# Kernel tuning notes

Hardware: AMD Instinct MI355X
Metric: run time of the kernel (lower is better)

## Reference

```python
import jax, jax.numpy as jnp
import numpy as np

N, E, D = 50000, 1000000, 64
EPS = 1e-5


def setup_inputs() -> dict:
    key = jax.random.key(0)
    ks = jax.random.split(key, 20)
    inp = {
        "x": jax.random.normal(ks[0], (N, D), dtype=jnp.float32),
        "e": jax.random.uniform(ks[1], (E,), dtype=jnp.float32),
        "edge_index": jax.random.randint(ks[2], (2, E), 0, N, dtype=jnp.int64),
    }
    dims = [(3 * D, D), (D, D), (D, D), (D, D)]
    for i, (fi, fo) in enumerate(dims):
        s = 1.0 / np.sqrt(fi)
        inp[f"W{i+1}"] = jax.random.uniform(ks[3 + 4 * i], (fi, fo), minval=-s, maxval=s, dtype=jnp.float32)
        inp[f"b{i+1}"] = jax.random.uniform(ks[4 + 4 * i], (fo,), minval=-s, maxval=s, dtype=jnp.float32)
        inp[f"g{i+1}"] = jnp.ones((fo,), dtype=jnp.float32)
        inp[f"bt{i+1}"] = jnp.zeros((fo,), dtype=jnp.float32)
    return inp


def _layer(h, W, b, g, bt):
    h = h @ W + b
    mu = jnp.mean(h, axis=-1, keepdims=True)
    var = jnp.mean(jnp.square(h - mu), axis=-1, keepdims=True)
    h = (h - mu) * jax.lax.rsqrt(var + EPS) * g + bt
    return jax.nn.relu(h)


def reference(x, e, edge_index, W1, b1, g1, bt1, W2, b2, g2, bt2, W3, b3, g3, bt3, W4, b4, g4, bt4):
    start, end = edge_index[0], edge_index[1]
    we = e[:, None]  # [E,1]
    # aggregate weighted neighbor features on each side
    mi = jax.ops.segment_sum(we * x[start], end, num_segments=x.shape[0])
    mo = jax.ops.segment_sum(we * x[end], start, num_segments=x.shape[0])
    h = jnp.concatenate([mi, mo, x], axis=1)  # [N, 3D]
    h = _layer(h, W1, b1, g1, bt1)
    h = _layer(h, W2, b2, g2, bt2)
    h = _layer(h, W3, b3, g3, bt3)
    h = _layer(h, W4, b4, g4, bt4)
    return h
```

## Files before the change

### kernel.cpp

```cpp
#include <hip/hip_runtime.h>

#define DD 64
#define EPSV 1e-5f

__device__ __forceinline__ float rlane_f(float v, int k) {
    return __int_as_float(__builtin_amdgcn_readlane(__float_as_int(v), k));
}

__global__ void detect_idx_kernel(const void* __restrict__ idx, int* __restrict__ flag,
                                  int nsample, int n_nodes) {
    const long long* p = (const long long*)idx;
    int bad = 0;
    for (int i = threadIdx.x; i < nsample; i += blockDim.x) {
        long long v = p[i];
        if (v < 0 || v >= (long long)n_nodes) bad = 1;
    }
    __shared__ int sbad;
    if (threadIdx.x == 0) sbad = 0;
    __syncthreads();
    if (bad) atomicOr(&sbad, 1);
    __syncthreads();
    if (threadIdx.x == 0) *flag = sbad ? 0 : 1;
}

__global__ __launch_bounds__(256) void hist_kernel(
    const void* __restrict__ idx, const int* __restrict__ flag,
    int* __restrict__ cnt0, int* __restrict__ cnt1, int n_edges) {
    const bool is64 = (*flag != 0);
    const long long* p64 = (const long long*)idx;
    const int*       p32 = (const int*)idx;
    int tid = blockIdx.x * blockDim.x + threadIdx.x;
    int stride = gridDim.x * blockDim.x;
    for (int ed = tid; ed < n_edges; ed += stride) {
        int s, t;
        if (is64) { s = (int)p64[ed]; t = (int)p64[n_edges + ed]; }
        else      { s = p32[ed];      t = p32[n_edges + ed]; }
        atomicAdd(&cnt0[t], 1);
        atomicAdd(&cnt1[s], 1);
    }
}

#define SC 52
__global__ __launch_bounds__(1024) void scan_kernel(
    const int* __restrict__ cnt0, const int* __restrict__ cnt1,
    int* __restrict__ offs0, int* __restrict__ offs1,
    int* __restrict__ cur0, int* __restrict__ cur1, int n) {
    const int* cnt = blockIdx.x ? cnt1 : cnt0;
    int* offs = blockIdx.x ? offs1 : offs0;
    int* cur  = blockIdx.x ? cur1  : cur0;
    const int t = threadIdx.x;
    const int base = t * SC;
    int m = n - base; if (m > SC) m = SC; if (m < 0) m = 0;

    int v[SC];
    int sum = 0;
    if (m == SC) {
        const int4* c4 = (const int4*)(cnt + base);
        #pragma unroll
        for (int i = 0; i < SC / 4; ++i) {
            int4 q = c4[i];
            v[4*i] = q.x; v[4*i+1] = q.y; v[4*i+2] = q.z; v[4*i+3] = q.w;
        }
        #pragma unroll
        for (int i = 0; i < SC; ++i) sum += v[i];
    } else {
        for (int i = 0; i < m; ++i) sum += cnt[base + i];
    }

    const int lane = t & 63, wid = t >> 6;
    int s = sum;
    #pragma unroll
    for (int d = 1; d < 64; d <<= 1) { int u = __shfl_up(s, d, 64); if (lane >= d) s += u; }

    __shared__ int wtot[16];
    if (lane == 63) wtot[wid] = s;
    __syncthreads();
    if (t < 16) {
        int w = wtot[t];
        int sw = w;
        #pragma unroll
        for (int d = 1; d < 16; d <<= 1) { int u = __shfl_up(sw, d, 64); if (t >= d) sw += u; }
        wtot[t] = sw - w;
    }
    __syncthreads();

    int run = wtot[wid] + (s - sum);
    if (m == SC) {
        int4* o4 = (int4*)(offs + base);
        int4* c4w = (int4*)(cur + base);
        #pragma unroll
        for (int i = 0; i < SC / 4; ++i) {
            int4 q;
            q.x = run; run += v[4*i];
            q.y = run; run += v[4*i+1];
            q.z = run; run += v[4*i+2];
            q.w = run; run += v[4*i+3];
            o4[i] = q; c4w[i] = q;
        }
        if (base + SC == n) offs[n] = run;
    } else if (m > 0) {
        for (int i = 0; i < m; ++i) {
            int c = cnt[base + i];
            offs[base + i] = run;
            cur[base + i]  = run;
            run += c;
        }
        if (base + m == n) offs[n] = run;
    }
}

__global__ __launch_bounds__(256) void fill_kernel(
    const void* __restrict__ idx, const float* __restrict__ e, const int* __restrict__ flag,
    int* __restrict__ cur0, int* __restrict__ cur1,
    int2* __restrict__ pay0, int2* __restrict__ pay1, int n_edges) {
    const bool is64 = (*flag != 0);
    const long long* p64 = (const long long*)idx;
    const int*       p32 = (const int*)idx;
    int tid = blockIdx.x * blockDim.x + threadIdx.x;
    int stride = gridDim.x * blockDim.x;
    for (int ed = tid; ed < n_edges; ed += stride) {
        int s, t;
        if (is64) { s = (int)p64[ed]; t = (int)p64[n_edges + ed]; }
        else      { s = p32[ed];      t = p32[n_edges + ed]; }
        int wbits = __float_as_int(e[ed]);
        int p0 = atomicAdd(&cur0[t], 1);
        pay0[p0] = make_int2(s, wbits);
        int p1 = atomicAdd(&cur1[s], 1);
        pay1[p1] = make_int2(t, wbits);
    }
}

__global__ __launch_bounds__(256) void gather_kernel(
    const float* __restrict__ x,
    const int2* __restrict__ pay0, const int2* __restrict__ pay1,
    const int* __restrict__ offs0, const int* __restrict__ offs1,
    float* __restrict__ mi, float* __restrict__ mo, int n) {
    const int wid = threadIdx.x >> 6, lane = threadIdx.x & 63;
    const int gid = blockIdx.x * 4 + wid;
    if (gid >= 2 * n) return;
    const int dir = gid & 1, node = gid >> 1;
    const int* offs = dir ? offs1 : offs0;
    const int2* pay = dir ? pay1 : pay0;
    float* dst = dir ? mo : mi;

    const int o0 = offs[node], o1 = offs[node + 1];
    float acc = 0.0f;
    for (int b = o0; b < o1; b += 64) {
        int2 pl = make_int2(0, 0);
        if (b + lane < o1) pl = pay[b + lane];
        const int cnt = min(64, o1 - b);
        #pragma unroll 4
        for (int j = 0; j < cnt; ++j) {
            int src  = __builtin_amdgcn_readlane(pl.x, j);
            float w  = __int_as_float(__builtin_amdgcn_readlane(pl.y, j));
            acc = fmaf(w, x[src * DD + lane], acc);
        }
    }
    dst[node * DD + lane] = acc;
}

__global__ __launch_bounds__(256) void scatter_kernel(
    const float* __restrict__ x, const float* __restrict__ e,
    const void* __restrict__ idx, const int* __restrict__ flag,
    float* __restrict__ mi, float* __restrict__ mo, int n_edges) {
    const int lane  = threadIdx.x & 63;
    const int slot  = (blockIdx.x * blockDim.x + threadIdx.x) >> 6;
    const int nslot = (gridDim.x * blockDim.x) >> 6;
    const bool is64 = (*flag != 0);
    const long long* p64 = (const long long*)idx;
    const int*       p32 = (const int*)idx;
    for (int ed = slot; ed < n_edges; ed += nslot) {
        int s, t;
        if (is64) { s = (int)p64[ed]; t = (int)p64[n_edges + ed]; }
        else      { s = p32[ed];      t = p32[n_edges + ed]; }
        float w  = e[ed];
        unsafeAtomicAdd(&mi[t * DD + lane], w * x[s * DD + lane]);
        unsafeAtomicAdd(&mo[s * DD + lane], w * x[t * DD + lane]);
    }
}

#define NPW 13

template<int N>
__device__ __forceinline__ void accumG(const float* __restrict__ wcol,
                                       const float (&h)[N], float (&acc)[N]) {
    #pragma unroll 8
    for (int k = 0; k < 64; ++k) {
        float w = wcol[k * 64];
        #pragma unroll
        for (int m = 0; m < N; ++m) acc[m] = fmaf(w, rlane_f(h[m], k), acc[m]);
    }
}

__device__ __forceinline__ float ln_relu(float v, float g, float bt) {
    float s = v;
    #pragma unroll
    for (int off = 32; off; off >>= 1) s += __shfl_xor(s, off, 64);
    float mu = s * (1.0f / 64.0f);
    float d = v - mu;
    float s2 = d * d;
    #pragma unroll
    for (int off = 32; off; off >>= 1) s2 += __shfl_xor(s2, off, 64);
    float r = d * rsqrtf(s2 * (1.0f / 64.0f) + EPSV) * g + bt;
    return fmaxf(r, 0.0f);
}

__global__ __launch_bounds__(512) void fused_mlp4(
    const float* __restrict__ mi, const float* __restrict__ mo, const float* __restrict__ x,
    const float* __restrict__ W1, const float* __restrict__ b1, const float* __restrict__ g1, const float* __restrict__ bt1,
    const float* __restrict__ W2, const float* __restrict__ b2, const float* __restrict__ g2, const float* __restrict__ bt2,
    const float* __restrict__ W3, const float* __restrict__ b3, const float* __restrict__ g3, const float* __restrict__ bt3,
    const float* __restrict__ W4, const float* __restrict__ b4, const float* __restrict__ g4, const float* __restrict__ bt4,
    float* __restrict__ out, int n_nodes) {

    const int wid = threadIdx.x >> 6, lane = threadIdx.x & 63;
    const int gw = blockIdx.x * 8 + wid;
    const int ngroups = (n_nodes + NPW - 1) / NPW;
    if (gw >= ngroups) return;
    const int n0 = gw * NPW;

    float hmi[NPW], hmo[NPW], hx[NPW];
    #pragma unroll
    for (int m = 0; m < NPW; ++m) {
        int n = n0 + m; if (n >= n_nodes) n = n_nodes - 1;
        hmi[m] = mi[n * DD + lane];
        hmo[m] = mo[n * DD + lane];
        hx[m]  = x[n * DD + lane];
    }

    float acc[NPW], h[NPW];

    {
        float bj = b1[lane];
        #pragma unroll
        for (int m = 0; m < NPW; ++m) acc[m] = bj;
        accumG(W1 + lane,             hmi, acc);
        accumG(W1 + 64 * DD + lane,   hmo, acc);
        accumG(W1 + 128 * DD + lane,  hx,  acc);
        float gj = g1[lane], btj = bt1[lane];
        #pragma unroll
        for (int m = 0; m < NPW; ++m) h[m] = ln_relu(acc[m], gj, btj);
    }

    {
        float bj = b2[lane];
        #pragma unroll
        for (int m = 0; m < NPW; ++m) acc[m] = bj;
        accumG(W2 + lane, h, acc);
        float gj = g2[lane], btj = bt2[lane];
        #pragma unroll
        for (int m = 0; m < NPW; ++m) h[m] = ln_relu(acc[m], gj, btj);
    }
    {
        float bj = b3[lane];
        #pragma unroll
        for (int m = 0; m < NPW; ++m) acc[m] = bj;
        accumG(W3 + lane, h, acc);
        float gj = g3[lane], btj = bt3[lane];
        #pragma unroll
        for (int m = 0; m < NPW; ++m) h[m] = ln_relu(acc[m], gj, btj);
    }
    {
        float bj = b4[lane];
        #pragma unroll
        for (int m = 0; m < NPW; ++m) acc[m] = bj;
        accumG(W4 + lane, h, acc);
        float gj = g4[lane], btj = bt4[lane];
        #pragma unroll
        for (int m = 0; m < NPW; ++m) h[m] = ln_relu(acc[m], gj, btj);
    }

    #pragma unroll
    for (int m = 0; m < NPW; ++m) {
        int n = n0 + m;
        if (n < n_nodes) out[n * DD + lane] = h[m];
    }
}

extern "C" void kernel_launch(void* const* d_in, const int* in_sizes, int n_in,
                              void* d_out, int out_size, void* d_ws, size_t ws_size,
                              hipStream_t stream) {
    const float* x   = (const float*)d_in[0];
    const float* e   = (const float*)d_in[1];
    const void*  idx = d_in[2];
    const float* W1 = (const float*)d_in[3],  *b1 = (const float*)d_in[4],
               * g1 = (const float*)d_in[5],  *bt1 = (const float*)d_in[6];
    const float* W2 = (const float*)d_in[7],  *b2 = (const float*)d_in[8],
               * g2 = (const float*)d_in[9],  *bt2 = (const float*)d_in[10];
    const float* W3 = (const float*)d_in[11], *b3 = (const float*)d_in[12],
               * g3 = (const float*)d_in[13], *bt3 = (const float*)d_in[14];
    const float* W4 = (const float*)d_in[15], *b4 = (const float*)d_in[16],
               * g4 = (const float*)d_in[17], *bt4 = (const float*)d_in[18];
    float* out = (float*)d_out;

    const int n_nodes = in_sizes[0] / DD;
    const int n_edges = in_sizes[1];

    float* mi = (float*)d_ws;
    float* mo = mi + (size_t)n_nodes * DD;
    int*  flag = (int*)(mo + (size_t)n_nodes * DD);
    char* p = (char*)(flag + 4);
    const int offs_pad = (n_nodes + 1 + 3) & ~3;
    int2* pay0 = (int2*)p;            p += (size_t)n_edges * sizeof(int2);
    int2* pay1 = (int2*)p;            p += (size_t)n_edges * sizeof(int2);
    int* cnt0  = (int*)p;             p += (size_t)n_nodes * 4;
    int* cnt1  = (int*)p;             p += (size_t)n_nodes * 4;
    int* offs0 = (int*)p;             p += (size_t)offs_pad * 4;
    int* offs1 = (int*)p;             p += (size_t)offs_pad * 4;
    int* cur0  = (int*)p;             p += (size_t)n_nodes * 4;
    int* cur1  = (int*)p;             p += (size_t)n_nodes * 4;
    const size_t need = (size_t)(p - (char*)d_ws);

    detect_idx_kernel<<<1, 256, 0, stream>>>(idx, flag, 4096, n_nodes);

    if (ws_size >= need) {
        hipMemsetAsync(cnt0, 0, (size_t)2 * n_nodes * 4, stream);
        hist_kernel<<<2048, 256, 0, stream>>>(idx, flag, cnt0, cnt1, n_edges);
        scan_kernel<<<2, 1024, 0, stream>>>(cnt0, cnt1, offs0, offs1, cur0, cur1, n_nodes);
        fill_kernel<<<2048, 256, 0, stream>>>(idx, e, flag, cur0, cur1, pay0, pay1, n_edges);
        const int nblocks = (2 * n_nodes + 3) / 4;
        gather_kernel<<<nblocks, 256, 0, stream>>>(x, pay0, pay1, offs0, offs1, mi, mo, n_nodes);
    } else {
        hipMemsetAsync(d_ws, 0, (size_t)2 * n_nodes * DD * sizeof(float), stream);
        scatter_kernel<<<4096, 256, 0, stream>>>(x, e, idx, flag, mi, mo, n_edges);
    }

    const int ngroups = (n_nodes + NPW - 1) / NPW;
    const int mblocks = (ngroups + 7) / 8;
    fused_mlp4<<<mblocks, 512, 0, stream>>>(
        mi, mo, x,
        W1, b1, g1, bt1, W2, b2, g2, bt2, W3, b3, g3, bt3, W4, b4, g4, bt4,
        out, n_nodes);
}
```

Measured before the change: 604.3 us.

## Replace per-node CSR build with coarse node bins and LDS atomic accumulation

Edges are bucketed into bins of 256 destination nodes, with a shared-memory histogram, a tiny scan, and an atomic append into one payload array carrying the local node index. Each bin is then reduced by a workgroup into a 64KB LDS tile using shared-memory float atomics and written out. This removes the per-node scan and the per-node counters, but it adds heavy global atomic contention on a few hundred bin cursors and LDS atomic traffic. The 64KB LDS tile limits occupancy, and summation order becomes nondeterministic.

```diff
diff --git a/kernel.cpp b/kernel.cpp
--- a/kernel.cpp
+++ b/kernel.cpp
@@ -2,6 +2,8 @@
 
 #define DD 64
 #define EPSV 1e-5f
+#define BINSZ 256
+#define NBINMAX 256
 
 __device__ __forceinline__ float rlane_f(float v, int k) {
     return __int_as_float(__builtin_amdgcn_readlane(__float_as_int(v), k));
@@ -23,140 +25,109 @@
     if (threadIdx.x == 0) *flag = sbad ? 0 : 1;
 }
 
-__global__ __launch_bounds__(256) void hist_kernel(
+__global__ __launch_bounds__(512) void binhist_kernel(
     const void* __restrict__ idx, const int* __restrict__ flag,
-    int* __restrict__ cnt0, int* __restrict__ cnt1, int n_edges) {
+    int* __restrict__ cnt, int nbin, int n_edges) {
+    __shared__ int h[2 * NBINMAX];
+    const int tid = threadIdx.x;
+    for (int i = tid; i < 2 * nbin; i += 512) h[i] = 0;
+    __syncthreads();
     const bool is64 = (*flag != 0);
     const long long* p64 = (const long long*)idx;
     const int*       p32 = (const int*)idx;
-    int tid = blockIdx.x * blockDim.x + threadIdx.x;
-    int stride = gridDim.x * blockDim.x;
-    for (int ed = tid; ed < n_edges; ed += stride) {
+    int gid = blockIdx.x * 512 + tid;
+    int stride = gridDim.x * 512;
+    for (int ed = gid; ed < n_edges; ed += stride) {
         int s, t;
         if (is64) { s = (int)p64[ed]; t = (int)p64[n_edges + ed]; }
         else      { s = p32[ed];      t = p32[n_edges + ed]; }
-        atomicAdd(&cnt0[t], 1);
-        atomicAdd(&cnt1[s], 1);
-    }
-}
-
-#define SC 52
-__global__ __launch_bounds__(1024) void scan_kernel(
-    const int* __restrict__ cnt0, const int* __restrict__ cnt1,
-    int* __restrict__ offs0, int* __restrict__ offs1,
-    int* __restrict__ cur0, int* __restrict__ cur1, int n) {
-    const int* cnt = blockIdx.x ? cnt1 : cnt0;
-    int* offs = blockIdx.x ? offs1 : offs0;
-    int* cur  = blockIdx.x ? cur1  : cur0;
+        atomicAdd(&h[t >> 8], 1);
+        atomicAdd(&h[nbin + (s >> 8)], 1);
+    }
+    __syncthreads();
+    for (int i = tid; i < 2 * nbin; i += 512) {
+        int v = h[i];
+        if (v) atomicAdd(&cnt[i], v);
+    }
+}
+
+__global__ void binscan_kernel(const int* __restrict__ cnt,
+                               int* __restrict__ base, int* __restrict__ cur, int nb) {
     const int t = threadIdx.x;
-    const int base = t * SC;
-    int m = n - base; if (m > SC) m = SC; if (m < 0) m = 0;
-
-    int v[SC];
+    const int C = (nb + 63) >> 6;
+    const int b0 = t * C;
+    int m = nb - b0; if (m > C) m = C; if (m < 0) m = 0;
+    int v[8];
     int sum = 0;
-    if (m == SC) {
-        const int4* c4 = (const int4*)(cnt + base);
-        #pragma unroll
-        for (int i = 0; i < SC / 4; ++i) {
-            int4 q = c4[i];
-            v[4*i] = q.x; v[4*i+1] = q.y; v[4*i+2] = q.z; v[4*i+3] = q.w;
-        }
-        #pragma unroll
-        for (int i = 0; i < SC; ++i) sum += v[i];
-    } else {
-        for (int i = 0; i < m; ++i) sum += cnt[base + i];
-    }
-
-    const int lane = t & 63, wid = t >> 6;
+    for (int i = 0; i < m; ++i) { v[i] = cnt[b0 + i]; sum += v[i]; }
     int s = sum;
     #pragma unroll
-    for (int d = 1; d < 64; d <<= 1) { int u = __shfl_up(s, d, 64); if (lane >= d) s += u; }
-
-    __shared__ int wtot[16];
-    if (lane == 63) wtot[wid] = s;
-    __syncthreads();
-    if (t < 16) {
-        int w = wtot[t];
-        int sw = w;
-        #pragma unroll
-        for (int d = 1; d < 16; d <<= 1) { int u = __shfl_up(sw, d, 64); if (t >= d) sw += u; }
-        wtot[t] = sw - w;
-    }
-    __syncthreads();
-
-    int run = wtot[wid] + (s - sum);
-    if (m == SC) {
-        int4* o4 = (int4*)(offs + base);
-        int4* c4w = (int4*)(cur + base);
-        #pragma unroll
-        for (int i = 0; i < SC / 4; ++i) {
-            int4 q;
-            q.x = run; run += v[4*i];
-            q.y = run; run += v[4*i+1];
-            q.z = run; run += v[4*i+2];
-            q.w = run; run += v[4*i+3];
-            o4[i] = q; c4w[i] = q;
-        }
-        if (base + SC == n) offs[n] = run;
-    } else if (m > 0) {
-        for (int i = 0; i < m; ++i) {
-            int c = cnt[base + i];
-            offs[base + i] = run;
-            cur[base + i]  = run;
-            run += c;
-        }
-        if (base + m == n) offs[n] = run;
-    }
-}
-
-__global__ __launch_bounds__(256) void fill_kernel(
+    for (int d = 1; d < 64; d <<= 1) { int u = __shfl_up(s, d, 64); if (t >= d) s += u; }
+    int run = s - sum;
+    for (int i = 0; i < m; ++i) {
+        base[b0 + i] = run;
+        cur[b0 + i]  = run;
+        run += v[i];
+    }
+}
+
+__global__ __launch_bounds__(256) void binscatter_kernel(
     const void* __restrict__ idx, const float* __restrict__ e, const int* __restrict__ flag,
-    int* __restrict__ cur0, int* __restrict__ cur1,
-    int2* __restrict__ pay0, int2* __restrict__ pay1, int n_edges) {
+    int* __restrict__ cur, int2* __restrict__ pay, int nbin, int n_edges) {
     const bool is64 = (*flag != 0);
     const long long* p64 = (const long long*)idx;
     const int*       p32 = (const int*)idx;
-    int tid = blockIdx.x * blockDim.x + threadIdx.x;
-    int stride = gridDim.x * blockDim.x;
-    for (int ed = tid; ed < n_edges; ed += stride) {
+    int gid = blockIdx.x * 256 + threadIdx.x;
+    int stride = gridDim.x * 256;
+    for (int ed = gid; ed < n_edges; ed += stride) {
         int s, t;
         if (is64) { s = (int)p64[ed]; t = (int)p64[n_edges + ed]; }
         else      { s = p32[ed];      t = p32[n_edges + ed]; }
         int wbits = __float_as_int(e[ed]);
-        int p0 = atomicAdd(&cur0[t], 1);
-        pay0[p0] = make_int2(s, wbits);
-        int p1 = atomicAdd(&cur1[s], 1);
-        pay1[p1] = make_int2(t, wbits);
-    }
-}
-
-__global__ __launch_bounds__(256) void gather_kernel(
-    const float* __restrict__ x,
-    const int2* __restrict__ pay0, const int2* __restrict__ pay1,
-    const int* __restrict__ offs0, const int* __restrict__ offs1,
-    float* __restrict__ mi, float* __restrict__ mo, int n) {
-    const int wid = threadIdx.x >> 6, lane = threadIdx.x & 63;
-    const int gid = blockIdx.x * 4 + wid;
-    if (gid >= 2 * n) return;
-    const int dir = gid & 1, node = gid >> 1;
-    const int* offs = dir ? offs1 : offs0;
-    const int2* pay = dir ? pay1 : pay0;
+        int slot0 = atomicAdd(&cur[t >> 8], 1);
+        pay[slot0] = make_int2(s | ((t & 255) << 16), wbits);
+        int slot1 = atomicAdd(&cur[nbin + (s >> 8)], 1);
+        pay[slot1] = make_int2(t | ((s & 255) << 16), wbits);
+    }
+}
+
+__global__ __launch_bounds__(512) void binacc_kernel(
+    const float* __restrict__ x, const int2* __restrict__ pay,
+    const int* __restrict__ base, const int* __restrict__ cnt,
+    float* __restrict__ mi, float* __restrict__ mo, int nbin, int n_nodes) {
+    __shared__ float acc[BINSZ * DD];
+    const int tid = threadIdx.x;
+    const int wg = blockIdx.x;
+    const int dir = (wg >= nbin) ? 1 : 0;
+    const int bin = dir ? wg - nbin : wg;
+
+    for (int i = tid; i < BINSZ * DD; i += 512) acc[i] = 0.0f;
+    __syncthreads();
+
+    const int b0 = base[wg], c = cnt[wg];
+    const int lane = tid & 63, wv = tid >> 6;
+
+    for (int off = wv * 64; off < c; off += 512) {
+        int2 pl = make_int2(0, 0);
+        if (off + lane < c) pl = pay[b0 + off + lane];
+        const int m = min(64, c - off);
+        #pragma unroll 4
+        for (int j = 0; j < m; ++j) {
+            int   meta = __builtin_amdgcn_readlane(pl.x, j);
+            float w    = __int_as_float(__builtin_amdgcn_readlane(pl.y, j));
+            int src = meta & 0xFFFF;
+            int tl  = (meta >> 16) & 0xFF;
+            atomicAdd(&acc[tl * DD + lane], w * x[src * DD + lane]);
+        }
+    }
+    __syncthreads();
+
     float* dst = dir ? mo : mi;
-
-    const int o0 = offs[node], o1 = offs[node + 1];
-    float acc = 0.0f;
-    for (int b = o0; b < o1; b += 64) {
-        int2 pl = make_int2(0, 0);
-        if (b + lane < o1) pl = pay[b + lane];
-        const int cnt = min(64, o1 - b);
-        #pragma unroll 4
-        for (int j = 0; j < cnt; ++j) {
-            int src  = __builtin_amdgcn_readlane(pl.x, j);
-            float w  = __int_as_float(__builtin_amdgcn_readlane(pl.y, j));
-            acc = fmaf(w, x[src * DD + lane], acc);
-        }
-    }
-    dst[node * DD + lane] = acc;
+    const int node0 = bin * BINSZ;
+    int nfl = (n_nodes - node0);
+    if (nfl > BINSZ) nfl = BINSZ;
+    nfl *= DD;
+    for (int i = tid; i < nfl; i += 512) dst[node0 * DD + i] = acc[i];
 }
 
 __global__ __launch_bounds__(256) void scatter_kernel(
@@ -241,7 +212,6 @@
         #pragma unroll
         for (int m = 0; m < NPW; ++m) h[m] = ln_relu(acc[m], gj, btj);
     }
-
     {
         float bj = b2[lane];
         #pragma unroll
@@ -295,31 +265,26 @@
 
     const int n_nodes = in_sizes[0] / DD;
     const int n_edges = in_sizes[1];
+    const int nbin = (n_nodes + BINSZ - 1) / BINSZ;
 
     float* mi = (float*)d_ws;
     float* mo = mi + (size_t)n_nodes * DD;
     int*  flag = (int*)(mo + (size_t)n_nodes * DD);
     char* p = (char*)(flag + 4);
-    const int offs_pad = (n_nodes + 1 + 3) & ~3;
-    int2* pay0 = (int2*)p;            p += (size_t)n_edges * sizeof(int2);
-    int2* pay1 = (int2*)p;            p += (size_t)n_edges * sizeof(int2);
-    int* cnt0  = (int*)p;             p += (size_t)n_nodes * 4;
-    int* cnt1  = (int*)p;             p += (size_t)n_nodes * 4;
-    int* offs0 = (int*)p;             p += (size_t)offs_pad * 4;
-    int* offs1 = (int*)p;             p += (size_t)offs_pad * 4;
-    int* cur0  = (int*)p;             p += (size_t)n_nodes * 4;
-    int* cur1  = (int*)p;             p += (size_t)n_nodes * 4;
+    int2* pay = (int2*)p;             p += (size_t)2 * n_edges * sizeof(int2);
+    int* cnt  = (int*)p;              p += (size_t)2 * nbin * 4;
+    int* base = (int*)p;              p += (size_t)2 * nbin * 4;
+    int* cur  = (int*)p;              p += (size_t)2 * nbin * 4;
     const size_t need = (size_t)(p - (char*)d_ws);
 
     detect_idx_kernel<<<1, 256, 0, stream>>>(idx, flag, 4096, n_nodes);
 
-    if (ws_size >= need) {
-        hipMemsetAsync(cnt0, 0, (size_t)2 * n_nodes * 4, stream);
-        hist_kernel<<<2048, 256, 0, stream>>>(idx, flag, cnt0, cnt1, n_edges);
-        scan_kernel<<<2, 1024, 0, stream>>>(cnt0, cnt1, offs0, offs1, cur0, cur1, n_nodes);
-        fill_kernel<<<2048, 256, 0, stream>>>(idx, e, flag, cur0, cur1, pay0, pay1, n_edges);
-        const int nblocks = (2 * n_nodes + 3) / 4;
-        gather_kernel<<<nblocks, 256, 0, stream>>>(x, pay0, pay1, offs0, offs1, mi, mo, n_nodes);
+    if (ws_size >= need && n_nodes <= 65535 && nbin <= NBINMAX) {
+        hipMemsetAsync(cnt, 0, (size_t)2 * nbin * 4, stream);
+        binhist_kernel<<<1024, 512, 0, stream>>>(idx, flag, cnt, nbin, n_edges);
+        binscan_kernel<<<1, 64, 0, stream>>>(cnt, base, cur, 2 * nbin);
+        binscatter_kernel<<<2048, 256, 0, stream>>>(idx, e, flag, cur, pay, nbin, n_edges);
+        binacc_kernel<<<2 * nbin, 512, 0, stream>>>(x, pay, base, cnt, mi, mo, nbin, n_nodes);
     } else {
         hipMemsetAsync(d_ws, 0, (size_t)2 * n_nodes * DD * sizeof(float), stream);
         scatter_kernel<<<4096, 256, 0, stream>>>(x, e, idx, flag, mi, mo, n_edges);
```

New measurement: 1.792 ms. 2.97x slower.
